# Optimization experiments

Hardware: AMD Instinct MI355X
Metric: run time of the kernel (lower is better)

## Reference

```python
import jax, jax.numpy as jnp
import numpy as np

NEG_INF = float(np.finfo(np.float32).min)
EPS = 1e-6
NOISE_STD = 1.0
CHUNK = 8
TEMP = 1.0


def moving_sum(x, back, forward):
    # x: [B, T]; windowed sum over [t-back, t+forward] via prefix sums (O(T))
    B, T = x.shape
    cs = jnp.concatenate([jnp.zeros((B, 1), x.dtype), jnp.cumsum(x, axis=1)], axis=1)  # [B, T+1]
    idx = jnp.arange(T)
    hi = jnp.clip(idx + forward + 1, 0, T)
    lo = jnp.clip(idx - back, 0, T)
    return cs[:, hi] - cs[:, lo]


def setup_inputs() -> dict:
    key = jax.random.key(0)
    ks = jax.random.split(key, 12)
    B, T, KD, QD, AD, VD = 16, 4000, 512, 512, 512, 512
    s = lambda d: 1.0 / np.sqrt(d)
    return {
        "key": jax.random.normal(ks[0], (B, T, KD), jnp.float32),
        "value": jax.random.normal(ks[1], (B, T, VD), jnp.float32),
        "query": jax.random.normal(ks[2], (B, 1, QD), jnp.float32),
        "mask": jnp.ones((B, 1, T), jnp.int32),
        "w_key_mono": jax.random.normal(ks[3], (KD, AD), jnp.float32) * s(KD),
        "b_key_mono": jnp.zeros((AD,), jnp.float32),
        "w_query_mono": jax.random.normal(ks[4], (QD, AD), jnp.float32) * s(QD),
        "v_mono": jax.random.normal(ks[5], (AD,), jnp.float32) * s(AD),
        "g_mono": jnp.asarray(np.sqrt(1.0 / AD), jnp.float32),  # weight_norm gain init
        "r_mono": jnp.asarray(-4.0, jnp.float32),
        "w_key_chunk": jax.random.normal(ks[6], (KD, AD), jnp.float32) * s(KD),
        "b_key_chunk": jnp.zeros((AD,), jnp.float32),
        "w_query_chunk": jax.random.normal(ks[7], (QD, AD), jnp.float32) * s(QD),
        "v_chunk": jax.random.normal(ks[8], (AD,), jnp.float32) * s(AD),
    }


def _energy(key, query, mask, wk, bk, wq, v, r=None, g=None):
    kproj = jax.nn.relu(key) @ wk + bk          # [B, T, A]
    qproj = query @ wq                           # [B, 1, A]
    if g is not None:  # weight-normalized v
        v = g * v / jnp.linalg.norm(v)
    e = jnp.tanh(kproj + qproj) @ v              # [B, T]
    if r is not None:
        e = e + r
    return jnp.where(mask[:, 0, :] == 0, NEG_INF, e)


def reference(key, value, query, mask, w_key_mono, b_key_mono, w_query_mono, v_mono,
              g_mono, r_mono, w_key_chunk, b_key_chunk, w_query_chunk, v_chunk):
    B, T, _ = key.shape
    e_mono = _energy(key, query, mask, w_key_mono, b_key_mono, w_query_mono,
                     v_mono, r=r_mono, g=g_mono)
    noise = jax.random.normal(jax.random.key(123), e_mono.shape, e_mono.dtype) * NOISE_STD
    p_choose = jax.nn.sigmoid(e_mono + noise)                      # [B, T]
    # safe_cumprod of (1 - p): exp(exclusive cumsum of clipped logs)
    log1mp = jnp.log(jnp.clip(1.0 - p_choose, EPS, 1.0))
    cumprod_1mp = jnp.exp(jnp.cumsum(log1mp, axis=1) - log1mp)     # exclusive
    aw_prev = jnp.zeros((B, T), key.dtype).at[:, 0].set(1.0)       # one-hot at t=0
    alpha = p_choose * cumprod_1mp * jnp.cumsum(
        aw_prev / jnp.clip(cumprod_1mp, EPS, 1.0), axis=1)
    # chunkwise attention
    e_chunk = _energy(key, query, mask, w_key_chunk, b_key_chunk, w_query_chunk, v_chunk)
    e_chunk = e_chunk - jnp.max(e_chunk, axis=1, keepdims=True)
    softmax_exp = jnp.maximum(jnp.exp(e_chunk), 1e-5)
    denom = moving_sum(softmax_exp, CHUNK - 1, 0)
    beta = softmax_exp * moving_sum(alpha * TEMP / denom, 0, CHUNK - 1)
    cv = jnp.einsum('bt,btd->bd', beta, value)[:, None, :]         # [B, 1, V]
    return cv, alpha[..., None]
```

## Files before the change

### kernel.cpp

```cpp
#include <hip/hip_runtime.h>
#include <stdint.h>

typedef unsigned short u16;
typedef unsigned int   u32;

#define T_LEN 4000
#define NEG_INF (-3.4028234663852886e38f)

typedef __bf16 bf16x8 __attribute__((ext_vector_type(8)));
typedef float  f32x4  __attribute__((ext_vector_type(4)));

__device__ __forceinline__ u16 f2bf(float f){
    union { float f; u32 i; } v; v.f = f;
    u32 u = v.i;
    u32 r = (u + 0x7FFFu + ((u >> 16) & 1u)) >> 16;
    return (u16)r;
}
__device__ __forceinline__ float tanh_fast(float x){
    float ax = fabsf(x);
    float a = __expf(-2.0f * ax);
    float t = (1.0f - a) / (1.0f + a);
    return copysignf(t, x);
}
__device__ __forceinline__ u32 rotl32(u32 x, int n){ return (x << n) | (x >> (32 - n)); }

__device__ __forceinline__ void gll16(const void* g, void* l){
    __builtin_amdgcn_global_load_lds(
        (__attribute__((address_space(1))) void*)g,
        (__attribute__((address_space(3))) void*)l, 16, 0, 0);
}

__device__ float jax_noise(u32 idx){
    const u32 k0 = 0u, k1 = 123u;
    const u32 k2 = k0 ^ k1 ^ 0x1BD11BDAu;
    u32 x0 = k0;
    u32 x1 = idx + k1;
#define RND(r) { x0 += x1; x1 = rotl32(x1, r); x1 ^= x0; }
    RND(13) RND(15) RND(26) RND(6)   x0 += k1; x1 += k2 + 1u;
    RND(17) RND(29) RND(16) RND(24)  x0 += k2; x1 += k0 + 2u;
    RND(13) RND(15) RND(26) RND(6)   x0 += k0; x1 += k1 + 3u;
    RND(17) RND(29) RND(16) RND(24)  x0 += k1; x1 += k2 + 4u;
    RND(13) RND(15) RND(26) RND(6)   x0 += k2; x1 += k0 + 5u;
#undef RND
    u32 bits = x0 ^ x1;
    union { u32 i; float f; } u;
    u.i = (bits >> 9) | 0x3F800000u;
    float f01 = u.f - 1.0f;
    const float minval = -0.99999994f;
    float uu = f01 * (1.0f - minval) + minval;
    uu = fmaxf(uu, minval);
    return 1.41421356f * erfinvf(uu);
}

__global__ __launch_bounds__(512) void prep_combined(
    const float* __restrict__ v_mono, const float* __restrict__ g_mono,
    const float* __restrict__ query, const float* __restrict__ wq_mono,
    const float* __restrict__ wq_chunk,
    const float* __restrict__ wk_mono, const float* __restrict__ wk_chunk,
    const float* __restrict__ key,
    float* __restrict__ vn, float* __restrict__ qp_mono, float* __restrict__ qp_chunk,
    u16* __restrict__ Wt, u16* __restrict__ kb,
    float* __restrict__ ezero, float* __restrict__ outcv)
{
    __shared__ float shf[512];
    __shared__ u16 tile[32][33];
    const int blk = blockIdx.x;
    const int tid = threadIdx.x;
    if (blk == 0){
        float v = v_mono[tid];
        shf[tid] = v * v;
        __syncthreads();
        for (int off = 256; off >= 1; off >>= 1){
            if (tid < off) shf[tid] += shf[tid + off];
            __syncthreads();
        }
        float g = g_mono[0];
        vn[tid] = g * v / sqrtf(shf[0]);
    } else if (blk <= 32){
        int b = (blk - 1) >> 1;
        int which = (blk - 1) & 1;
        const float* W = which ? wq_chunk : wq_mono;
        float* out = which ? qp_chunk : qp_mono;
        shf[tid] = query[b * 512 + tid];
        __syncthreads();
        float acc = 0.f;
        for (int k = 0; k < 512; k++) acc += shf[k] * W[k * 512 + tid];
        out[b * 512 + tid] = acc;
    } else if (blk <= 544){
        int idx = blk - 33;
        int kt = (idx & 15) * 32, nt = (idx >> 4) * 32;
        int c = tid & 31, r = tid >> 5;
        const float* src = (nt < 512) ? wk_mono : wk_chunk;
        int nbase = (nt < 512) ? nt : nt - 512;
#pragma unroll
        for (int i = 0; i < 2; i++){
            int kk = r + i * 16;
            tile[kk][c] = f2bf(src[(size_t)(kt + kk) * 512 + nbase + c]);
        }
        __syncthreads();
#pragma unroll
        for (int i = 0; i < 2; i++){
            int nn = r + i * 16;
            Wt[(size_t)(nt + nn) * 512 + kt + c] = tile[c][nn];
        }
    } else if (blk < 608){
        int i = ((blk - 545) * 512 + tid) * 4;
        if (i < 128000){
            float4 z = {0.f, 0.f, 0.f, 0.f};
            *reinterpret_cast<float4*>(ezero + i) = z;
        }
    } else if (blk < 612){
        int i = ((blk - 608) * 512 + tid) * 4;
        float4 z = {0.f, 0.f, 0.f, 0.f};
        *reinterpret_cast<float4*>(outcv + i) = z;
    } else {
        size_t i = ((size_t)(blk - 612) * 512 + tid) * 8;
        float4 a = *reinterpret_cast<const float4*>(key + i);
        float4 b = *reinterpret_cast<const float4*>(key + i + 4);
        uint4 pk;
        pk.x = (u32)f2bf(fmaxf(a.x, 0.f)) | ((u32)f2bf(fmaxf(a.y, 0.f)) << 16);
        pk.y = (u32)f2bf(fmaxf(a.z, 0.f)) | ((u32)f2bf(fmaxf(a.w, 0.f)) << 16);
        pk.z = (u32)f2bf(fmaxf(b.x, 0.f)) | ((u32)f2bf(fmaxf(b.y, 0.f)) << 16);
        pk.w = (u32)f2bf(fmaxf(b.z, 0.f)) | ((u32)f2bf(fmaxf(b.w, 0.f)) << 16);
        *reinterpret_cast<uint4*>(kb + i) = pk;
    }
}

__global__ __launch_bounds__(256) void gemm_energy_pre(
    const u16* __restrict__ kb, const u16* __restrict__ Wt,
    const float* __restrict__ b_mono, const float* __restrict__ b_chunk,
    const float* __restrict__ vnorm, const float* __restrict__ v_chunk,
    const float* __restrict__ qp_mono, const float* __restrict__ qp_chunk,
    float* __restrict__ e_mono, float* __restrict__ e_chunk)
{
    __shared__ __align__(16) u16 As[2][128 * 64];
    __shared__ __align__(16) u16 Bs[2][128 * 64];
    const int bid = blockIdx.x;
    const int x = ((bid >> 6) << 3) + (bid & 7);
    if (x >= 500) return;
    const int nT = (bid >> 3) & 7;
    const int g0 = x * 128;
    const bool mono = (nT < 4);
    const int n0 = nT * 128;
    const int tid = threadIdx.x;
    const int lane = tid & 63;
    const int wave = tid >> 6;
    const int wm = wave >> 1, wn = wave & 1;
    const int l15 = lane & 15, quad = lane >> 4;

    f32x4 acc[4][4];
#pragma unroll
    for (int i = 0; i < 4; i++)
#pragma unroll
        for (int j = 0; j < 4; j++)
#pragma unroll
            for (int c = 0; c < 4; c++) acc[i][j][c] = 0.f;

    const u16* aG = kb + (size_t)g0 * 512;
    const u16* bG = Wt + (size_t)n0 * 512;

#define STAGE(bsel, k0) do{                                                     \
    _Pragma("unroll") for (int it_ = 0; it_ < 4; it_++){                        \
        int vid = tid + it_ * 256;                                              \
        int row = vid >> 3;                                                     \
        int sl  = (vid & 7) ^ (row & 7);                                        \
        gll16(aG + (size_t)row * 512 + (k0) + sl * 8, &As[bsel][vid * 8]);      \
        gll16(bG + (size_t)row * 512 + (k0) + sl * 8, &Bs[bsel][vid * 8]);      \
    }                                                                           \
}while(0)

    STAGE(0, 0);
    __syncthreads();

#pragma unroll 1
    for (int kt = 0; kt < 8; kt++){
        const int cur = kt & 1;
        if (kt < 7) STAGE(cur ^ 1, (kt + 1) * 64);
        bf16x8 af[4][2], bfr[4][2];
#pragma unroll
        for (int i = 0; i < 4; i++)
#pragma unroll
            for (int ks = 0; ks < 2; ks++){
                int ra = wm * 64 + i * 16 + l15;
                af[i][ks]  = *reinterpret_cast<const bf16x8*>(
                    &As[cur][ra * 64 + (((ks * 4 + quad) ^ (ra & 7)) << 3)]);
                int rb = wn * 64 + i * 16 + l15;
                bfr[i][ks] = *reinterpret_cast<const bf16x8*>(
                    &Bs[cur][rb * 64 + (((ks * 4 + quad) ^ (rb & 7)) << 3)]);
            }
#pragma unroll
        for (int i = 0; i < 4; i++)
#pragma unroll
            for (int j = 0; j < 4; j++)
#pragma unroll
                for (int ks = 0; ks < 2; ks++)
                    acc[i][j] = __builtin_amdgcn_mfma_f32_16x16x32_bf16(
                        af[i][ks], bfr[j][ks], acc[i][j], 0, 0, 0);
        __syncthreads();
    }
#undef STAGE

    const float* qp = mono ? qp_mono : qp_chunk;
    float* edst = mono ? e_mono : e_chunk;
    float vv[4], bb[4]; int nc[4];
#pragma unroll
    for (int j = 0; j < 4; j++){
        int ncol = (n0 - (mono ? 0 : 512)) + wn * 64 + j * 16 + l15;
        nc[j] = ncol;
        vv[j] = mono ? vnorm[ncol] : v_chunk[ncol];
        bb[j] = mono ? b_mono[ncol] : b_chunk[ncol];
    }
#pragma unroll
    for (int i = 0; i < 4; i++){
#pragma unroll
        for (int r = 0; r < 4; r++){
            int g = g0 + wm * 64 + i * 16 + quad * 4 + r;
            int bidx = (u32)g / 4000u;
            float s = 0.f;
#pragma unroll
            for (int j = 0; j < 4; j++){
                float x2 = acc[i][j][r] + bb[j] + qp[bidx * 512 + nc[j]];
                s += vv[j] * tanh_fast(x2);
            }
            s += __shfl_xor(s, 1);
            s += __shfl_xor(s, 2);
            s += __shfl_xor(s, 4);
            s += __shfl_xor(s, 8);
            if (l15 == 0) atomicAdd(&edst[g], s);
        }
    }
}

__global__ __launch_bounds__(256) void gemm_energy_f32(
    const float* __restrict__ key, const u16* __restrict__ Wt,
    const float* __restrict__ b_mono, const float* __restrict__ b_chunk,
    const float* __restrict__ vnorm, const float* __restrict__ v_chunk,
    const float* __restrict__ qp_mono, const float* __restrict__ qp_chunk,
    float* __restrict__ e_mono, float* __restrict__ e_chunk)
{
    __shared__ __align__(16) u16 As[128 * 40];
    __shared__ __align__(16) u16 Bs[128 * 40];
    const int tid = threadIdx.x;
    const int g0 = blockIdx.x * 128;
    const int nT = blockIdx.y;
    const bool mono = (nT < 4);
    const int n0 = nT * 128;
    const int lane = tid & 63;
    const int wave = tid >> 6;
    const int wm = wave >> 1, wn = wave & 1;
    const int l15 = lane & 15, quad = lane >> 4;

    f32x4 acc[4][4];
#pragma unroll
    for (int i = 0; i < 4; i++)
#pragma unroll
        for (int j = 0; j < 4; j++)
#pragma unroll
            for (int c = 0; c < 4; c++) acc[i][j][c] = 0.f;

    for (int k0 = 0; k0 < 512; k0 += 32){
        __syncthreads();
#pragma unroll
        for (int it = 0; it < 4; it++){
            int vid = tid + it * 256;
            int row = vid >> 3;
            int c4  = (vid & 7) << 2;
            float4 a = *reinterpret_cast<const float4*>(key + (size_t)(g0 + row) * 512 + k0 + c4);
            u32 p0 = (u32)f2bf(fmaxf(a.x, 0.f)) | ((u32)f2bf(fmaxf(a.y, 0.f)) << 16);
            u32 p1 = (u32)f2bf(fmaxf(a.z, 0.f)) | ((u32)f2bf(fmaxf(a.w, 0.f)) << 16);
            uint2 pk; pk.x = p0; pk.y = p1;
            *reinterpret_cast<uint2*>(&As[row * 40 + c4]) = pk;
        }
#pragma unroll
        for (int it = 0; it < 2; it++){
            int vid = tid + it * 256;
            int row = vid >> 2;
            int cb  = (vid & 3) << 3;
            uint4 b = *reinterpret_cast<const uint4*>(Wt + (size_t)(n0 + row) * 512 + k0 + cb);
            *reinterpret_cast<uint4*>(&Bs[row * 40 + cb]) = b;
        }
        __syncthreads();
        bf16x8 af[4], bfr[4];
#pragma unroll
        for (int i = 0; i < 4; i++){
            af[i]  = *reinterpret_cast<const bf16x8*>(&As[(wm * 64 + i * 16 + l15) * 40 + quad * 8]);
            bfr[i] = *reinterpret_cast<const bf16x8*>(&Bs[(wn * 64 + i * 16 + l15) * 40 + quad * 8]);
        }
#pragma unroll
        for (int i = 0; i < 4; i++)
#pragma unroll
            for (int j = 0; j < 4; j++)
                acc[i][j] = __builtin_amdgcn_mfma_f32_16x16x32_bf16(af[i], bfr[j], acc[i][j], 0, 0, 0);
    }

    const float* qp = mono ? qp_mono : qp_chunk;
    float* edst = mono ? e_mono : e_chunk;
    float vv[4], bb[4]; int nc[4];
#pragma unroll
    for (int j = 0; j < 4; j++){
        int ncol = (n0 - (mono ? 0 : 512)) + wn * 64 + j * 16 + l15;
        nc[j] = ncol;
        vv[j] = mono ? vnorm[ncol] : v_chunk[ncol];
        bb[j] = mono ? b_mono[ncol] : b_chunk[ncol];
    }
#pragma unroll
    for (int i = 0; i < 4; i++){
#pragma unroll
        for (int r = 0; r < 4; r++){
            int g = g0 + wm * 64 + i * 16 + quad * 4 + r;
            int bidx = (u32)g / 4000u;
            float s = 0.f;
#pragma unroll
            for (int j = 0; j < 4; j++){
                float x = acc[i][j][r] + bb[j] + qp[bidx * 512 + nc[j]];
                s += vv[j] * tanh_fast(x);
            }
            s += __shfl_xor(s, 1);
            s += __shfl_xor(s, 2);
            s += __shfl_xor(s, 4);
            s += __shfl_xor(s, 8);
            if (l15 == 0) atomicAdd(&edst[g], s);
        }
    }
}

#define IDX(t) ((t) + ((t) >> 4))

__global__ __launch_bounds__(512) void scan_energy(
    const float* __restrict__ e_mono, const float* __restrict__ e_chunk,
    const int* __restrict__ mask, const float* __restrict__ r_mono,
    float* __restrict__ out_alpha, float* __restrict__ beta)
{
    __shared__ float P[4256];
    __shared__ float AL[4256];
    __shared__ float SE[4256];
    __shared__ float red[512];
    const int b = blockIdx.x;
    const int tid = threadIdx.x;
    const float r = r_mono[0];
    const int t0 = tid * 8;

    float l[8];
    float lsum = 0.f;
#pragma unroll
    for (int i = 0; i < 8; i++){
        int t = t0 + i;
        if (t < T_LEN){
            int fl = b * T_LEN + t;
            float e = e_mono[fl] + r;
            if (mask[fl] == 0) e = NEG_INF;
            float x = e + jax_noise((u32)fl);
            float p = 1.0f / (1.0f + expf(-x));
            P[IDX(t)] = p;
            float om = 1.0f - p;
            om = fminf(fmaxf(om, 1e-6f), 1.0f);
            l[i] = logf(om);
            lsum += l[i];
        } else l[i] = 0.f;
    }
    red[tid] = lsum;
    __syncthreads();
#pragma unroll
    for (int off = 1; off < 512; off <<= 1){
        float v = (tid >= off) ? red[tid - off] : 0.f;
        __syncthreads();
        red[tid] += v;
        __syncthreads();
    }
    float run = red[tid] - lsum;
#pragma unroll
    for (int i = 0; i < 8; i++){
        int t = t0 + i;
        if (t < T_LEN){
            float alpha = P[IDX(t)] * expf(run);
            run += l[i];
            AL[IDX(t)] = alpha;
            out_alpha[b * T_LEN + t] = alpha;
        }
    }

    float ec[8]; float lmax = NEG_INF;
#pragma unroll
    for (int i = 0; i < 8; i++){
        int t = t0 + i;
        if (t < T_LEN){
            int fl = b * T_LEN + t;
            float e = e_chunk[fl];
            if (mask[fl] == 0) e = NEG_INF;
            ec[i] = e;
            lmax = fmaxf(lmax, e);
        } else ec[i] = NEG_INF;
    }
    __syncthreads();
    red[tid] = lmax;
    __syncthreads();
    for (int off = 256; off >= 1; off >>= 1){
        if (tid < off) red[tid] = fmaxf(red[tid], red[tid + off]);
        __syncthreads();
    }
    float m = red[0];
#pragma unroll
    for (int i = 0; i < 8; i++){
        int t = t0 + i;
        if (t < T_LEN) SE[IDX(t)] = fmaxf(expf(ec[i] - m), 1e-5f);
    }
    __syncthreads();
#pragma unroll
    for (int i = 0; i < 8; i++){
        int t = t0 + i;
        if (t < T_LEN){
            float d = 0.f;
            int lo = t - 7; if (lo < 0) lo = 0;
            for (int s = lo; s <= t; s++) d += SE[IDX(s)];
            P[IDX(t)] = AL[IDX(t)] / d;
        }
    }
    __syncthreads();
#pragma unroll
    for (int i = 0; i < 8; i++){
        int t = t0 + i;
        if (t < T_LEN){
            float s2 = 0.f;
            int hi = t + 7; if (hi > T_LEN - 1) hi = T_LEN - 1;
            for (int s = t; s <= hi; s++) s2 += P[IDX(s)];
            beta[b * T_LEN + t] = SE[IDX(t)] * s2;
        }
    }
}

__global__ __launch_bounds__(256) void cv_accum(const float* __restrict__ value,
                                                const float* __restrict__ beta,
                                                float* __restrict__ outcv){
    const int b = blockIdx.x >> 5;
    const int c = blockIdx.x & 31;
    const int tid = threadIdx.x;
    __shared__ float bsh[125];
    __shared__ float part[512];
    int tstart = c * 125;
    if (tid < 125) bsh[tid] = beta[b * T_LEN + tstart + tid];
    __syncthreads();
    int dl = (tid & 127) * 4;
    int trow = tid >> 7;
    float4 a = {0.f, 0.f, 0.f, 0.f};
    for (int t = trow; t < 125; t += 2){
        float bt = bsh[t];
        float4 v = *reinterpret_cast<const float4*>(
            value + (size_t)(b * T_LEN + tstart + t) * 512 + dl);
        a.x += bt * v.x; a.y += bt * v.y; a.z += bt * v.z; a.w += bt * v.w;
    }
    if (trow == 1){
        part[(tid & 127) * 4 + 0] = a.x;
        part[(tid & 127) * 4 + 1] = a.y;
        part[(tid & 127) * 4 + 2] = a.z;
        part[(tid & 127) * 4 + 3] = a.w;
    }
    __syncthreads();
    if (trow == 0){
        a.x += part[(tid & 127) * 4 + 0];
        a.y += part[(tid & 127) * 4 + 1];
        a.z += part[(tid & 127) * 4 + 2];
        a.w += part[(tid & 127) * 4 + 3];
        atomicAdd(&outcv[b * 512 + dl + 0], a.x);
        atomicAdd(&outcv[b * 512 + dl + 1], a.y);
        atomicAdd(&outcv[b * 512 + dl + 2], a.z);
        atomicAdd(&outcv[b * 512 + dl + 3], a.w);
    }
}

extern "C" void kernel_launch(void* const* d_in, const int* in_sizes, int n_in,
                              void* d_out, int out_size, void* d_ws, size_t ws_size,
                              hipStream_t stream)
{
    const float* key      = (const float*)d_in[0];
    const float* value    = (const float*)d_in[1];
    const float* query    = (const float*)d_in[2];
    const int*   mask     = (const int*)d_in[3];
    const float* wk_mono  = (const float*)d_in[4];
    const float* bk_mono  = (const float*)d_in[5];
    const float* wq_mono  = (const float*)d_in[6];
    const float* v_mono   = (const float*)d_in[7];
    const float* g_mono   = (const float*)d_in[8];
    const float* r_mono   = (const float*)d_in[9];
    const float* wk_chunk = (const float*)d_in[10];
    const float* bk_chunk = (const float*)d_in[11];
    const float* wq_chunk = (const float*)d_in[12];
    const float* v_chunk  = (const float*)d_in[13];

    float* ws      = (float*)d_ws;
    float* e_mono  = ws;
    float* e_chunk = ws + 64000;
    float* beta    = ws + 136192;
    float* qp_mono = ws + 200192;
    float* qp_chunk= ws + 208384;
    float* vnorm   = ws + 216576;
    u16*   Wt      = (u16*)(ws + 217088);
    u16*   kb      = (u16*)(ws + 479232);

    const size_t NEED = 479232u * 4u + (size_t)64000 * 512 * 2;
    const bool big = ws_size >= NEED;

    prep_combined<<<big ? 8612 : 612, 512, 0, stream>>>(
        v_mono, g_mono, query, wq_mono, wq_chunk, wk_mono, wk_chunk, key,
        vnorm, qp_mono, qp_chunk, Wt, kb, e_mono, (float*)d_out);

    if (big){
        gemm_energy_pre<<<4096, 256, 0, stream>>>(kb, Wt, bk_mono, bk_chunk,
                                                  vnorm, v_chunk, qp_mono, qp_chunk,
                                                  e_mono, e_chunk);
    } else {
        gemm_energy_f32<<<dim3(500, 8), 256, 0, stream>>>(key, Wt, bk_mono, bk_chunk,
                                                          vnorm, v_chunk, qp_mono, qp_chunk,
                                                          e_mono, e_chunk);
    }
    scan_energy<<<16, 512, 0, stream>>>(e_mono, e_chunk, mask, r_mono,
                                        (float*)d_out + 8192, beta);
    cv_accum<<<512, 256, 0, stream>>>(value, beta, (float*)d_out);
}
```

Baseline: 454.0 us.

## Enlarge GEMM tile to 256x256 with 1024-thread blocks and LDS partial reduction

Reworks the energy GEMM from 128x128 tiles with 256 threads to 256x256 tiles with 16 waves per block. This halves operand reloads per output and reduces global atomics by summing per-wave partial energies in LDS before a single atomicAdd per row. It also hoists the query-projection loads for the at most two batches a tile spans and uses a new block-index swizzle. LDS use grows to about 132KB per block, which limits occupancy to one block per CU, and the larger tiles leave fewer blocks to cover load latency.

Measured after the change: 431.2 us. 5.0% less time.

```diff
diff --git a/kernel.cpp b/kernel.cpp
--- a/kernel.cpp
+++ b/kernel.cpp
@@ -126,26 +126,29 @@
     }
 }
 
-__global__ __launch_bounds__(256) void gemm_energy_pre(
+__global__ __launch_bounds__(1024) void gemm_energy_pre(
     const u16* __restrict__ kb, const u16* __restrict__ Wt,
     const float* __restrict__ b_mono, const float* __restrict__ b_chunk,
     const float* __restrict__ vnorm, const float* __restrict__ v_chunk,
     const float* __restrict__ qp_mono, const float* __restrict__ qp_chunk,
     float* __restrict__ e_mono, float* __restrict__ e_chunk)
 {
-    __shared__ __align__(16) u16 As[2][128 * 64];
-    __shared__ __align__(16) u16 Bs[2][128 * 64];
+    __shared__ __align__(16) u16 As[2][256 * 64];
+    __shared__ __align__(16) u16 Bs[2][256 * 64];
+    __shared__ float part[4][256];
+
     const int bid = blockIdx.x;
-    const int x = ((bid >> 6) << 3) + (bid & 7);
-    if (x >= 500) return;
-    const int nT = (bid >> 3) & 7;
-    const int g0 = x * 128;
-    const bool mono = (nT < 4);
-    const int n0 = nT * 128;
+    const int swz = (bid & 7) * 125 + (bid >> 3);
+    const int xt = swz >> 2;
+    const int nT = swz & 3;
+    const int g0 = xt * 256;
+    const int n0 = nT * 256;
+    const bool mono = (nT < 2);
+
     const int tid = threadIdx.x;
     const int lane = tid & 63;
     const int wave = tid >> 6;
-    const int wm = wave >> 1, wn = wave & 1;
+    const int wm = wave >> 2, wn = wave & 3;
     const int l15 = lane & 15, quad = lane >> 4;
 
     f32x4 acc[4][4];
@@ -160,8 +163,8 @@
     const u16* bG = Wt + (size_t)n0 * 512;
 
 #define STAGE(bsel, k0) do{                                                     \
-    _Pragma("unroll") for (int it_ = 0; it_ < 4; it_++){                        \
-        int vid = tid + it_ * 256;                                              \
+    _Pragma("unroll") for (int it_ = 0; it_ < 2; it_++){                        \
+        int vid = tid + it_ * 1024;                                             \
         int row = vid >> 3;                                                     \
         int sl  = (vid & 7) ^ (row & 7);                                        \
         gll16(aG + (size_t)row * 512 + (k0) + sl * 8, &As[bsel][vid * 8]);      \
@@ -176,58 +179,69 @@
     for (int kt = 0; kt < 8; kt++){
         const int cur = kt & 1;
         if (kt < 7) STAGE(cur ^ 1, (kt + 1) * 64);
-        bf16x8 af[4][2], bfr[4][2];
-#pragma unroll
-        for (int i = 0; i < 4; i++)
-#pragma unroll
-            for (int ks = 0; ks < 2; ks++){
+#pragma unroll
+        for (int ks = 0; ks < 2; ks++){
+            bf16x8 af[4], bf[4];
+#pragma unroll
+            for (int i = 0; i < 4; i++){
                 int ra = wm * 64 + i * 16 + l15;
-                af[i][ks]  = *reinterpret_cast<const bf16x8*>(
+                af[i] = *reinterpret_cast<const bf16x8*>(
                     &As[cur][ra * 64 + (((ks * 4 + quad) ^ (ra & 7)) << 3)]);
-                int rb = wn * 64 + i * 16 + l15;
-                bfr[i][ks] = *reinterpret_cast<const bf16x8*>(
+            }
+#pragma unroll
+            for (int j = 0; j < 4; j++){
+                int rb = wn * 64 + j * 16 + l15;
+                bf[j] = *reinterpret_cast<const bf16x8*>(
                     &Bs[cur][rb * 64 + (((ks * 4 + quad) ^ (rb & 7)) << 3)]);
             }
 #pragma unroll
-        for (int i = 0; i < 4; i++)
-#pragma unroll
-            for (int j = 0; j < 4; j++)
-#pragma unroll
-                for (int ks = 0; ks < 2; ks++)
+            for (int i = 0; i < 4; i++)
+#pragma unroll
+                for (int j = 0; j < 4; j++)
                     acc[i][j] = __builtin_amdgcn_mfma_f32_16x16x32_bf16(
-                        af[i][ks], bfr[j][ks], acc[i][j], 0, 0, 0);
+                        af[i], bf[j], acc[i][j], 0, 0, 0);
+        }
         __syncthreads();
     }
 #undef STAGE
 
     const float* qp = mono ? qp_mono : qp_chunk;
     float* edst = mono ? e_mono : e_chunk;
-    float vv[4], bb[4]; int nc[4];
+    const int b0 = g0 / 4000;
+    const int b1 = (g0 + 255) / 4000;
+    float vv[4], bb[4], qA[4], qB[4];
 #pragma unroll
     for (int j = 0; j < 4; j++){
-        int ncol = (n0 - (mono ? 0 : 512)) + wn * 64 + j * 16 + l15;
-        nc[j] = ncol;
-        vv[j] = mono ? vnorm[ncol] : v_chunk[ncol];
-        bb[j] = mono ? b_mono[ncol] : b_chunk[ncol];
+        int c = (n0 - (mono ? 0 : 512)) + wn * 64 + j * 16 + l15;
+        vv[j] = mono ? vnorm[c] : v_chunk[c];
+        bb[j] = mono ? b_mono[c] : b_chunk[c];
+        qA[j] = qp[b0 * 512 + c];
+        qB[j] = qp[b1 * 512 + c];
     }
 #pragma unroll
     for (int i = 0; i < 4; i++){
 #pragma unroll
         for (int r = 0; r < 4; r++){
-            int g = g0 + wm * 64 + i * 16 + quad * 4 + r;
-            int bidx = (u32)g / 4000u;
+            int rl = wm * 64 + i * 16 + quad * 4 + r;
+            int bidx = (u32)(g0 + rl) / 4000u;
             float s = 0.f;
 #pragma unroll
             for (int j = 0; j < 4; j++){
-                float x2 = acc[i][j][r] + bb[j] + qp[bidx * 512 + nc[j]];
-                s += vv[j] * tanh_fast(x2);
+                float x = acc[i][j][r] + bb[j] + (bidx == b0 ? qA[j] : qB[j]);
+                s += vv[j] * tanh_fast(x);
             }
             s += __shfl_xor(s, 1);
             s += __shfl_xor(s, 2);
             s += __shfl_xor(s, 4);
             s += __shfl_xor(s, 8);
-            if (l15 == 0) atomicAdd(&edst[g], s);
-        }
+            if (l15 == 0) part[wn][rl] = s;
+        }
+    }
+    __syncthreads();
+    if ((wave & 3) == 0){
+        int rl = wm * 64 + lane;
+        float t = part[0][rl] + part[1][rl] + part[2][rl] + part[3][rl];
+        atomicAdd(&edst[g0 + rl], t);
     }
 }
 
@@ -504,9 +518,9 @@
         vnorm, qp_mono, qp_chunk, Wt, kb, e_mono, (float*)d_out);
 
     if (big){
-        gemm_energy_pre<<<4096, 256, 0, stream>>>(kb, Wt, bk_mono, bk_chunk,
-                                                  vnorm, v_chunk, qp_mono, qp_chunk,
-                                                  e_mono, e_chunk);
+        gemm_energy_pre<<<1000, 1024, 0, stream>>>(kb, Wt, bk_mono, bk_chunk,
+                                                   vnorm, v_chunk, qp_mono, qp_chunk,
+                                                   e_mono, e_chunk);
     } else {
         gemm_energy_f32<<<dim3(500, 8), 256, 0, stream>>>(key, Wt, bk_mono, bk_chunk,
                                                           vnorm, v_chunk, qp_mono, qp_chunk,
```
